# Optimization experiments

Measured on AMD Instinct MI355X. Metric: run time of the kernel, lower is better.

The kernel has to match this reference:

```python
import jax, jax.numpy as jnp
import numpy as np

B = 8192
NUM_CLASSES = 1024
DELTA = 0.2
GAMMA_1 = 10.0
GAMMA_2 = 0.5


def setup_inputs() -> dict:
    key = jax.random.key(0)
    k1, k2 = jax.random.split(key)
    scores = jax.random.uniform(k1, (B, B), dtype=jnp.float32)
    targets = jax.random.randint(k2, (B,), 0, NUM_CLASSES, dtype=jnp.int64)
    return {"scores": scores, "targets": targets}


def _side_loss(S, mask):
    # S: [B, B] similarities for this direction; mask: [B, B] bool, True = same label (positive)
    neg_mask = ~mask
    neg_inf = jnp.float32(-jnp.inf)
    pos_inf = jnp.float32(jnp.inf)
    max_an = jnp.max(jnp.where(neg_mask, S, neg_inf), axis=1)  # [B] hardest-negative score
    min_ap = jnp.min(jnp.where(mask, S, pos_inf), axis=1)      # [B] weakest-positive score
    # informative-pair filters (per row)
    ap_pair = mask & (S < (max_an + DELTA)[:, None])
    an_pair = neg_mask & (S > (min_ap - DELTA)[:, None])
    # masked exp-sums (log-sum-exp style margin terms)
    pos_sum = jnp.sum(jnp.where(ap_pair, jnp.exp(GAMMA_2 - GAMMA_1 * S), 0.0), axis=1)
    neg_sum = jnp.sum(jnp.where(an_pair, jnp.exp(GAMMA_1 * S - GAMMA_2), 0.0), axis=1)
    # safe log: rows with empty pair sets are marked invalid and zeroed later
    pos_loss = jnp.log(jnp.where(pos_sum > 0, pos_sum, 1.0)) / GAMMA_1
    neg_loss = jnp.log(jnp.where(neg_sum > 0, neg_sum, 1.0)) / GAMMA_1
    valid = jnp.any(ap_pair, axis=1) & jnp.any(an_pair, axis=1)
    return pos_loss + neg_loss, valid


def reference(scores, targets):
    batch_size = scores.shape[0]
    mask = targets[:, None] == targets[None, :]  # symmetric label-equality mask
    cap_loss, cap_valid = _side_loss(scores, mask)        # caption retrieval rows
    im_loss, im_valid = _side_loss(scores.T, mask)        # image retrieval rows (mask is symmetric)
    valid = cap_valid & im_valid  # original skips row if ANY of the 4 pair sets is empty
    loss = jnp.sum(jnp.where(valid, cap_loss + im_loss, 0.0)) / batch_size
    return loss
```

## Files before the change

### kernel.cpp

```cpp
#include <hip/hip_runtime.h>
#include <cmath>

#define BB 8192
#define NCH 64

static constexpr float kG1 = 10.0f;
static constexpr float kG2 = 0.5f;
static constexpr float kDelta = 0.2f;

__device__ __forceinline__ float wsum(float v){
#pragma unroll
  for (int o = 32; o > 0; o >>= 1) v += __shfl_xor(v, o);
  return v;
}
__device__ __forceinline__ float wmaxr(float v){
#pragma unroll
  for (int o = 32; o > 0; o >>= 1) v = fmaxf(v, __shfl_xor(v, o));
  return v;
}
__device__ __forceinline__ float wminr(float v){
#pragma unroll
  for (int o = 32; o > 0; o >>= 1) v = fminf(v, __shfl_xor(v, o));
  return v;
}


__global__ __launch_bounds__(256) void k_init(int* __restrict__ wsi, float* __restrict__ out){
  int i = blockIdx.x * 256 + threadIdx.x;
  if (i < 2*BB)      wsi[i] = (int)0xFF800000u;
  else if (i < 4*BB) wsi[i] = 0x7F800000;
  else if (i < 8*BB) reinterpret_cast<float*>(wsi)[i] = 0.0f;
  if (i == 0) out[0] = 0.0f;
}

__global__ __launch_bounds__(256) void k_row_stats(const float* __restrict__ S,
                                                   const int* __restrict__ tg,
                                                   int* __restrict__ row_max,
                                                   int* __restrict__ row_min){
  const int r = blockIdx.x;
  const int tr = tg[r];
  const float4* row = reinterpret_cast<const float4*>(S + (size_t)r * BB);
  const int4*  t4  = reinterpret_cast<const int4*>(tg);
  float mx = -INFINITY, mn = INFINITY;
  for (int it = threadIdx.x; it < BB/4; it += 256){
    float4 v = row[it];
    int4   t = t4[it];
    if (t.x == tr) mn = fminf(mn, v.x); else mx = fmaxf(mx, v.x);
    if (t.y == tr) mn = fminf(mn, v.y); else mx = fmaxf(mx, v.y);
    if (t.z == tr) mn = fminf(mn, v.z); else mx = fmaxf(mx, v.z);
    if (t.w == tr) mn = fminf(mn, v.w); else mx = fmaxf(mx, v.w);
  }
  mx = wmaxr(mx); mn = wminr(mn);
  __shared__ float smx[4], smn[4];
  const int wid = threadIdx.x >> 6;
  if ((threadIdx.x & 63) == 0){ smx[wid] = mx; smn[wid] = mn; }
  __syncthreads();
  if (threadIdx.x == 0){
    float a = smx[0], b = smn[0];
#pragma unroll
    for (int w = 1; w < 4; ++w){ a = fmaxf(a, smx[w]); b = fminf(b, smn[w]); }
    row_max[r] = __float_as_int(a);
    row_min[r] = __float_as_int(b);
  }
}

__global__ __launch_bounds__(256) void k_row_sums(const float* __restrict__ S,
                                                  const int* __restrict__ tg,
                                                  const int* __restrict__ row_max,
                                                  const int* __restrict__ row_min,
                                                  float* __restrict__ row_pos,
                                                  float* __restrict__ row_neg){
  const int r = blockIdx.x;
  const int tr = tg[r];
  const float pth = __int_as_float(row_max[r]) + kDelta;
  const float nth = __int_as_float(row_min[r]) - kDelta;
  const float4* row = reinterpret_cast<const float4*>(S + (size_t)r * BB);
  const int4*  t4  = reinterpret_cast<const int4*>(tg);
  float pos = 0.f, neg = 0.f;
  for (int it = threadIdx.x; it < BB/4; it += 256){
    float4 v = row[it];
    int4   t = t4[it];
    if (t.x == tr){ if (v.x < pth) pos += __expf(kG2 - kG1 * v.x); }
    else          { if (v.x > nth) neg += __expf(kG1 * v.x - kG2); }
    if (t.y == tr){ if (v.y < pth) pos += __expf(kG2 - kG1 * v.y); }
    else          { if (v.y > nth) neg += __expf(kG1 * v.y - kG2); }
    if (t.z == tr){ if (v.z < pth) pos += __expf(kG2 - kG1 * v.z); }
    else          { if (v.z > nth) neg += __expf(kG1 * v.z - kG2); }
    if (t.w == tr){ if (v.w < pth) pos += __expf(kG2 - kG1 * v.w); }
    else          { if (v.w > nth) neg += __expf(kG1 * v.w - kG2); }
  }
  pos = wsum(pos); neg = wsum(neg);
  __shared__ float sp[4], sn[4];
  const int wid = threadIdx.x >> 6;
  if ((threadIdx.x & 63) == 0){ sp[wid] = pos; sn[wid] = neg; }
  __syncthreads();
  if (threadIdx.x == 0){
    float a = sp[0], b = sn[0];
#pragma unroll
    for (int w = 1; w < 4; ++w){ a += sp[w]; b += sn[w]; }
    row_pos[r] = a; row_neg[r] = b;
  }
}

__global__ __launch_bounds__(256) void k_col_stats(const float* __restrict__ S,
                                                   const int* __restrict__ tg,
                                                   int* __restrict__ col_max,
                                                   int* __restrict__ col_min){
  const int c = (blockIdx.x * 256 + threadIdx.x) * 4;
  const int4 tc = *reinterpret_cast<const int4*>(tg + c);
  const int r0 = blockIdx.y * (BB / NCH);
  const int r1 = r0 + (BB / NCH);
  float mx0=-INFINITY, mx1=-INFINITY, mx2=-INFINITY, mx3=-INFINITY;
  float mn0= INFINITY, mn1= INFINITY, mn2= INFINITY, mn3= INFINITY;
  for (int i = r0; i < r1; ++i){
    float4 v = *reinterpret_cast<const float4*>(S + (size_t)i * BB + c);
    const int ti = tg[i];
    if (ti == tc.x) mn0 = fminf(mn0, v.x); else mx0 = fmaxf(mx0, v.x);
    if (ti == tc.y) mn1 = fminf(mn1, v.y); else mx1 = fmaxf(mx1, v.y);
    if (ti == tc.z) mn2 = fminf(mn2, v.z); else mx2 = fmaxf(mx2, v.z);
    if (ti == tc.w) mn3 = fminf(mn3, v.w); else mx3 = fmaxf(mx3, v.w);
  }
  atomicMax(col_max + c + 0, __float_as_int(mx0));
  atomicMax(col_max + c + 1, __float_as_int(mx1));
  atomicMax(col_max + c + 2, __float_as_int(mx2));
  atomicMax(col_max + c + 3, __float_as_int(mx3));
  atomicMin(col_min + c + 0, __float_as_int(mn0));
  atomicMin(col_min + c + 1, __float_as_int(mn1));
  atomicMin(col_min + c + 2, __float_as_int(mn2));
  atomicMin(col_min + c + 3, __float_as_int(mn3));
}

__global__ __launch_bounds__(256) void k_col_sums(const float* __restrict__ S,
                                                  const int* __restrict__ tg,
                                                  const int* __restrict__ col_max,
                                                  const int* __restrict__ col_min,
                                                  float* __restrict__ col_pos,
                                                  float* __restrict__ col_neg){
  const int c = (blockIdx.x * 256 + threadIdx.x) * 4;
  const int4 tc = *reinterpret_cast<const int4*>(tg + c);
  const float pth0 = __int_as_float(col_max[c+0]) + kDelta;
  const float pth1 = __int_as_float(col_max[c+1]) + kDelta;
  const float pth2 = __int_as_float(col_max[c+2]) + kDelta;
  const float pth3 = __int_as_float(col_max[c+3]) + kDelta;
  const float nth0 = __int_as_float(col_min[c+0]) - kDelta;
  const float nth1 = __int_as_float(col_min[c+1]) - kDelta;
  const float nth2 = __int_as_float(col_min[c+2]) - kDelta;
  const float nth3 = __int_as_float(col_min[c+3]) - kDelta;
  const int r0 = blockIdx.y * (BB / NCH);
  const int r1 = r0 + (BB / NCH);
  float p0=0.f,p1=0.f,p2=0.f,p3=0.f, n0=0.f,n1=0.f,n2=0.f,n3=0.f;
  for (int i = r0; i < r1; ++i){
    float4 v = *reinterpret_cast<const float4*>(S + (size_t)i * BB + c);
    const int ti = tg[i];
    if (ti == tc.x){ if (v.x < pth0) p0 += __expf(kG2 - kG1 * v.x); }
    else           { if (v.x > nth0) n0 += __expf(kG1 * v.x - kG2); }
    if (ti == tc.y){ if (v.y < pth1) p1 += __expf(kG2 - kG1 * v.y); }
    else           { if (v.y > nth1) n1 += __expf(kG1 * v.y - kG2); }
    if (ti == tc.z){ if (v.z < pth2) p2 += __expf(kG2 - kG1 * v.z); }
    else           { if (v.z > nth2) n2 += __expf(kG1 * v.z - kG2); }
    if (ti == tc.w){ if (v.w < pth3) p3 += __expf(kG2 - kG1 * v.w); }
    else           { if (v.w > nth3) n3 += __expf(kG1 * v.w - kG2); }
  }
  atomicAdd(col_pos + c + 0, p0);
  atomicAdd(col_pos + c + 1, p1);
  atomicAdd(col_pos + c + 2, p2);
  atomicAdd(col_pos + c + 3, p3);
  atomicAdd(col_neg + c + 0, n0);
  atomicAdd(col_neg + c + 1, n1);
  atomicAdd(col_neg + c + 2, n2);
  atomicAdd(col_neg + c + 3, n3);
}

__global__ __launch_bounds__(256) void k_final(const float* __restrict__ row_pos,
                                               const float* __restrict__ row_neg,
                                               const float* __restrict__ col_pos,
                                               const float* __restrict__ col_neg,
                                               float* __restrict__ out){
  const int r = blockIdx.x * 256 + threadIdx.x;
  const float rp = row_pos[r], rn = row_neg[r];
  const float cp = col_pos[r], cn = col_neg[r];
  float l = 0.f;
  if (rp > 0.f && rn > 0.f && cp > 0.f && cn > 0.f)
    l = (logf(rp) + logf(rn) + logf(cp) + logf(cn)) * (1.0f / kG1);
  l = wsum(l);
  __shared__ float sm[4];
  const int wid = threadIdx.x >> 6;
  if ((threadIdx.x & 63) == 0) sm[wid] = l;
  __syncthreads();
  if (threadIdx.x == 0){
    float a = sm[0] + sm[1] + sm[2] + sm[3];
    atomicAdd(out, a * (1.0f / (float)BB));
  }
}

extern "C" void kernel_launch(void* const* d_in, const int* in_sizes, int n_in,
                              void* d_out, int out_size, void* d_ws, size_t ws_size,
                              hipStream_t stream) {
  const float* S  = (const float*)d_in[0];
  const int*   tg = (const int*)d_in[1];
  int*   wsi = (int*)d_ws;
  float* wsf = (float*)d_ws;
  int* row_max = wsi;
  int* col_max = wsi + BB;
  int* row_min = wsi + 2*BB;
  int* col_min = wsi + 3*BB;
  float* row_pos = wsf + 4*BB;
  float* row_neg = wsf + 5*BB;
  float* col_pos = wsf + 6*BB;
  float* col_neg = wsf + 7*BB;
  float* out = (float*)d_out;

  k_init<<<(8*BB)/256, 256, 0, stream>>>(wsi, out);
  k_row_stats<<<BB, 256, 0, stream>>>(S, tg, row_max, row_min);
  k_col_stats<<<dim3(BB/1024, NCH), 256, 0, stream>>>(S, tg, col_max, col_min);
  k_row_sums<<<BB, 256, 0, stream>>>(S, tg, row_max, row_min, row_pos, row_neg);
  k_col_sums<<<dim3(BB/1024, NCH), 256, 0, stream>>>(S, tg, col_max, col_min, col_pos, col_neg);
  k_final<<<BB/256, 256, 0, stream>>>(row_pos, row_neg, col_pos, col_neg, out);
}
```

Before: 523.9 us.

## Fuse row and column passes into shared tiled stats and sums kernels

Merges the separate row-wise and column-wise stat and sum kernels into two tiled kernels that read each matrix element once per phase. Row reductions are done per row with a wave shuffle and combined across waves and blocks with atomics, while column reductions stay in registers. This halves the number of full passes over the 8192x8192 matrix, at the cost of per-row shuffle reductions and many more global atomics. The exponential is also computed once per element and shared between the row and column sums.

```diff
diff --git a/kernel.cpp b/kernel.cpp
--- a/kernel.cpp
+++ b/kernel.cpp
@@ -2,7 +2,9 @@
 #include <cmath>
 
 #define BB 8192
-#define NCH 64
+#define RPB 64
+#define GY (BB / RPB)
+#define GX (BB / 1024)
 
 static constexpr float kG1 = 10.0f;
 static constexpr float kG2 = 0.5f;
@@ -11,16 +13,6 @@
 __device__ __forceinline__ float wsum(float v){
 #pragma unroll
   for (int o = 32; o > 0; o >>= 1) v += __shfl_xor(v, o);
-  return v;
-}
-__device__ __forceinline__ float wmaxr(float v){
-#pragma unroll
-  for (int o = 32; o > 0; o >>= 1) v = fmaxf(v, __shfl_xor(v, o));
-  return v;
-}
-__device__ __forceinline__ float wminr(float v){
-#pragma unroll
-  for (int o = 32; o > 0; o >>= 1) v = fminf(v, __shfl_xor(v, o));
   return v;
 }
 
@@ -33,142 +25,145 @@
   if (i == 0) out[0] = 0.0f;
 }
 
-__global__ __launch_bounds__(256) void k_row_stats(const float* __restrict__ S,
-                                                   const int* __restrict__ tg,
-                                                   int* __restrict__ row_max,
-                                                   int* __restrict__ row_min){
-  const int r = blockIdx.x;
-  const int tr = tg[r];
-  const float4* row = reinterpret_cast<const float4*>(S + (size_t)r * BB);
-  const int4*  t4  = reinterpret_cast<const int4*>(tg);
-  float mx = -INFINITY, mn = INFINITY;
-  for (int it = threadIdx.x; it < BB/4; it += 256){
-    float4 v = row[it];
-    int4   t = t4[it];
-    if (t.x == tr) mn = fminf(mn, v.x); else mx = fmaxf(mx, v.x);
-    if (t.y == tr) mn = fminf(mn, v.y); else mx = fmaxf(mx, v.y);
-    if (t.z == tr) mn = fminf(mn, v.z); else mx = fmaxf(mx, v.z);
-    if (t.w == tr) mn = fminf(mn, v.w); else mx = fmaxf(mx, v.w);
-  }
-  mx = wmaxr(mx); mn = wminr(mn);
-  __shared__ float smx[4], smn[4];
-  const int wid = threadIdx.x >> 6;
-  if ((threadIdx.x & 63) == 0){ smx[wid] = mx; smn[wid] = mn; }
-  __syncthreads();
-  if (threadIdx.x == 0){
-    float a = smx[0], b = smn[0];
-#pragma unroll
-    for (int w = 1; w < 4; ++w){ a = fmaxf(a, smx[w]); b = fminf(b, smn[w]); }
-    row_max[r] = __float_as_int(a);
-    row_min[r] = __float_as_int(b);
-  }
-}
-
-__global__ __launch_bounds__(256) void k_row_sums(const float* __restrict__ S,
-                                                  const int* __restrict__ tg,
-                                                  const int* __restrict__ row_max,
-                                                  const int* __restrict__ row_min,
-                                                  float* __restrict__ row_pos,
-                                                  float* __restrict__ row_neg){
-  const int r = blockIdx.x;
-  const int tr = tg[r];
-  const float pth = __int_as_float(row_max[r]) + kDelta;
-  const float nth = __int_as_float(row_min[r]) - kDelta;
-  const float4* row = reinterpret_cast<const float4*>(S + (size_t)r * BB);
-  const int4*  t4  = reinterpret_cast<const int4*>(tg);
-  float pos = 0.f, neg = 0.f;
-  for (int it = threadIdx.x; it < BB/4; it += 256){
-    float4 v = row[it];
-    int4   t = t4[it];
-    if (t.x == tr){ if (v.x < pth) pos += __expf(kG2 - kG1 * v.x); }
-    else          { if (v.x > nth) neg += __expf(kG1 * v.x - kG2); }
-    if (t.y == tr){ if (v.y < pth) pos += __expf(kG2 - kG1 * v.y); }
-    else          { if (v.y > nth) neg += __expf(kG1 * v.y - kG2); }
-    if (t.z == tr){ if (v.z < pth) pos += __expf(kG2 - kG1 * v.z); }
-    else          { if (v.z > nth) neg += __expf(kG1 * v.z - kG2); }
-    if (t.w == tr){ if (v.w < pth) pos += __expf(kG2 - kG1 * v.w); }
-    else          { if (v.w > nth) neg += __expf(kG1 * v.w - kG2); }
-  }
-  pos = wsum(pos); neg = wsum(neg);
-  __shared__ float sp[4], sn[4];
-  const int wid = threadIdx.x >> 6;
-  if ((threadIdx.x & 63) == 0){ sp[wid] = pos; sn[wid] = neg; }
-  __syncthreads();
-  if (threadIdx.x == 0){
-    float a = sp[0], b = sn[0];
-#pragma unroll
-    for (int w = 1; w < 4; ++w){ a += sp[w]; b += sn[w]; }
-    row_pos[r] = a; row_neg[r] = b;
-  }
-}
-
-__global__ __launch_bounds__(256) void k_col_stats(const float* __restrict__ S,
-                                                   const int* __restrict__ tg,
-                                                   int* __restrict__ col_max,
-                                                   int* __restrict__ col_min){
+__global__ __launch_bounds__(256) void k_stats(const float* __restrict__ S,
+                                               const int* __restrict__ tg,
+                                               int* __restrict__ row_max,
+                                               int* __restrict__ row_min,
+                                               int* __restrict__ col_max,
+                                               int* __restrict__ col_min){
   const int c = (blockIdx.x * 256 + threadIdx.x) * 4;
   const int4 tc = *reinterpret_cast<const int4*>(tg + c);
-  const int r0 = blockIdx.y * (BB / NCH);
-  const int r1 = r0 + (BB / NCH);
-  float mx0=-INFINITY, mx1=-INFINITY, mx2=-INFINITY, mx3=-INFINITY;
-  float mn0= INFINITY, mn1= INFINITY, mn2= INFINITY, mn3= INFINITY;
-  for (int i = r0; i < r1; ++i){
-    float4 v = *reinterpret_cast<const float4*>(S + (size_t)i * BB + c);
-    const int ti = tg[i];
-    if (ti == tc.x) mn0 = fminf(mn0, v.x); else mx0 = fmaxf(mx0, v.x);
-    if (ti == tc.y) mn1 = fminf(mn1, v.y); else mx1 = fmaxf(mx1, v.y);
-    if (ti == tc.z) mn2 = fminf(mn2, v.z); else mx2 = fmaxf(mx2, v.z);
-    if (ti == tc.w) mn3 = fminf(mn3, v.w); else mx3 = fmaxf(mx3, v.w);
-  }
-  atomicMax(col_max + c + 0, __float_as_int(mx0));
-  atomicMax(col_max + c + 1, __float_as_int(mx1));
-  atomicMax(col_max + c + 2, __float_as_int(mx2));
-  atomicMax(col_max + c + 3, __float_as_int(mx3));
-  atomicMin(col_min + c + 0, __float_as_int(mn0));
-  atomicMin(col_min + c + 1, __float_as_int(mn1));
-  atomicMin(col_min + c + 2, __float_as_int(mn2));
-  atomicMin(col_min + c + 3, __float_as_int(mn3));
-}
-
-__global__ __launch_bounds__(256) void k_col_sums(const float* __restrict__ S,
-                                                  const int* __restrict__ tg,
-                                                  const int* __restrict__ col_max,
-                                                  const int* __restrict__ col_min,
-                                                  float* __restrict__ col_pos,
-                                                  float* __restrict__ col_neg){
+  const int r0 = blockIdx.y * RPB;
+  const int lane = threadIdx.x & 63;
+
+  float cmx0=-INFINITY, cmx1=-INFINITY, cmx2=-INFINITY, cmx3=-INFINITY;
+  float cmn0= INFINITY, cmn1= INFINITY, cmn2= INFINITY, cmn3= INFINITY;
+
+  __shared__ int s_t[RPB];
+  if (threadIdx.x < RPB) s_t[threadIdx.x] = tg[r0 + threadIdx.x];
+  __syncthreads();
+
+#pragma unroll 2
+  for (int k = 0; k < RPB; ++k){
+    const int i = r0 + k;
+    const float4 v = *reinterpret_cast<const float4*>(S + (size_t)i * BB + c);
+    const int ti = s_t[k];
+    float rmx = -INFINITY, rmn = INFINITY;
+    if (ti == tc.x){ cmn0 = fminf(cmn0, v.x); rmn = fminf(rmn, v.x); }
+    else           { cmx0 = fmaxf(cmx0, v.x); rmx = fmaxf(rmx, v.x); }
+    if (ti == tc.y){ cmn1 = fminf(cmn1, v.y); rmn = fminf(rmn, v.y); }
+    else           { cmx1 = fmaxf(cmx1, v.y); rmx = fmaxf(rmx, v.y); }
+    if (ti == tc.z){ cmn2 = fminf(cmn2, v.z); rmn = fminf(rmn, v.z); }
+    else           { cmx2 = fmaxf(cmx2, v.z); rmx = fmaxf(rmx, v.z); }
+    if (ti == tc.w){ cmn3 = fminf(cmn3, v.w); rmn = fminf(rmn, v.w); }
+    else           { cmx3 = fmaxf(cmx3, v.w); rmx = fmaxf(rmx, v.w); }
+#pragma unroll
+    for (int o = 32; o > 0; o >>= 1){
+      rmx = fmaxf(rmx, __shfl_xor(rmx, o));
+      rmn = fminf(rmn, __shfl_xor(rmn, o));
+    }
+    if (lane == 0){
+      atomicMax(row_max + i, __float_as_int(rmx));
+      atomicMin(row_min + i, __float_as_int(rmn));
+    }
+  }
+  atomicMax(col_max + c + 0, __float_as_int(cmx0));
+  atomicMax(col_max + c + 1, __float_as_int(cmx1));
+  atomicMax(col_max + c + 2, __float_as_int(cmx2));
+  atomicMax(col_max + c + 3, __float_as_int(cmx3));
+  atomicMin(col_min + c + 0, __float_as_int(cmn0));
+  atomicMin(col_min + c + 1, __float_as_int(cmn1));
+  atomicMin(col_min + c + 2, __float_as_int(cmn2));
+  atomicMin(col_min + c + 3, __float_as_int(cmn3));
+}
+
+__global__ __launch_bounds__(256) void k_sums(const float* __restrict__ S,
+                                              const int* __restrict__ tg,
+                                              const int* __restrict__ row_max,
+                                              const int* __restrict__ row_min,
+                                              const int* __restrict__ col_max,
+                                              const int* __restrict__ col_min,
+                                              float* __restrict__ row_pos,
+                                              float* __restrict__ row_neg,
+                                              float* __restrict__ col_pos,
+                                              float* __restrict__ col_neg){
   const int c = (blockIdx.x * 256 + threadIdx.x) * 4;
   const int4 tc = *reinterpret_cast<const int4*>(tg + c);
-  const float pth0 = __int_as_float(col_max[c+0]) + kDelta;
-  const float pth1 = __int_as_float(col_max[c+1]) + kDelta;
-  const float pth2 = __int_as_float(col_max[c+2]) + kDelta;
-  const float pth3 = __int_as_float(col_max[c+3]) + kDelta;
-  const float nth0 = __int_as_float(col_min[c+0]) - kDelta;
-  const float nth1 = __int_as_float(col_min[c+1]) - kDelta;
-  const float nth2 = __int_as_float(col_min[c+2]) - kDelta;
-  const float nth3 = __int_as_float(col_min[c+3]) - kDelta;
-  const int r0 = blockIdx.y * (BB / NCH);
-  const int r1 = r0 + (BB / NCH);
-  float p0=0.f,p1=0.f,p2=0.f,p3=0.f, n0=0.f,n1=0.f,n2=0.f,n3=0.f;
-  for (int i = r0; i < r1; ++i){
-    float4 v = *reinterpret_cast<const float4*>(S + (size_t)i * BB + c);
-    const int ti = tg[i];
-    if (ti == tc.x){ if (v.x < pth0) p0 += __expf(kG2 - kG1 * v.x); }
-    else           { if (v.x > nth0) n0 += __expf(kG1 * v.x - kG2); }
-    if (ti == tc.y){ if (v.y < pth1) p1 += __expf(kG2 - kG1 * v.y); }
-    else           { if (v.y > nth1) n1 += __expf(kG1 * v.y - kG2); }
-    if (ti == tc.z){ if (v.z < pth2) p2 += __expf(kG2 - kG1 * v.z); }
-    else           { if (v.z > nth2) n2 += __expf(kG1 * v.z - kG2); }
-    if (ti == tc.w){ if (v.w < pth3) p3 += __expf(kG2 - kG1 * v.w); }
-    else           { if (v.w > nth3) n3 += __expf(kG1 * v.w - kG2); }
-  }
-  atomicAdd(col_pos + c + 0, p0);
-  atomicAdd(col_pos + c + 1, p1);
-  atomicAdd(col_pos + c + 2, p2);
-  atomicAdd(col_pos + c + 3, p3);
-  atomicAdd(col_neg + c + 0, n0);
-  atomicAdd(col_neg + c + 1, n1);
-  atomicAdd(col_neg + c + 2, n2);
-  atomicAdd(col_neg + c + 3, n3);
+  const int r0 = blockIdx.y * RPB;
+  const int lane = threadIdx.x & 63;
+
+  const float cpth0 = __int_as_float(col_max[c+0]) + kDelta;
+  const float cpth1 = __int_as_float(col_max[c+1]) + kDelta;
+  const float cpth2 = __int_as_float(col_max[c+2]) + kDelta;
+  const float cpth3 = __int_as_float(col_max[c+3]) + kDelta;
+  const float cnth0 = __int_as_float(col_min[c+0]) - kDelta;
+  const float cnth1 = __int_as_float(col_min[c+1]) - kDelta;
+  const float cnth2 = __int_as_float(col_min[c+2]) - kDelta;
+  const float cnth3 = __int_as_float(col_min[c+3]) - kDelta;
+
+  __shared__ int   s_t[RPB];
+  __shared__ float s_pth[RPB], s_nth[RPB];
+  if (threadIdx.x < RPB){
+    const int i = r0 + threadIdx.x;
+    s_t[threadIdx.x]   = tg[i];
+    s_pth[threadIdx.x] = __int_as_float(row_max[i]) + kDelta;
+    s_nth[threadIdx.x] = __int_as_float(row_min[i]) - kDelta;
+  }
+  __syncthreads();
+
+  float cp0=0.f,cp1=0.f,cp2=0.f,cp3=0.f, cn0=0.f,cn1=0.f,cn2=0.f,cn3=0.f;
+
+#pragma unroll 2
+  for (int k = 0; k < RPB; ++k){
+    const int i = r0 + k;
+    const float4 v = *reinterpret_cast<const float4*>(S + (size_t)i * BB + c);
+    const int   ti  = s_t[k];
+    const float rpth = s_pth[k], rnth = s_nth[k];
+    float rp = 0.f, rn = 0.f;
+
+    {
+      const bool pos = (ti == tc.x);
+      const float arg = kG1 * v.x - kG2;
+      const float e = __expf(pos ? -arg : arg);
+      if (pos){ if (v.x < rpth) rp += e;  if (v.x < cpth0) cp0 += e; }
+      else    { if (v.x > rnth) rn += e;  if (v.x > cnth0) cn0 += e; }
+    }
+    {
+      const bool pos = (ti == tc.y);
+      const float arg = kG1 * v.y - kG2;
+      const float e = __expf(pos ? -arg : arg);
+      if (pos){ if (v.y < rpth) rp += e;  if (v.y < cpth1) cp1 += e; }
+      else    { if (v.y > rnth) rn += e;  if (v.y > cnth1) cn1 += e; }
+    }
+    {
+      const bool pos = (ti == tc.z);
+      const float arg = kG1 * v.z - kG2;
+      const float e = __expf(pos ? -arg : arg);
+      if (pos){ if (v.z < rpth) rp += e;  if (v.z < cpth2) cp2 += e; }
+      else    { if (v.z > rnth) rn += e;  if (v.z > cnth2) cn2 += e; }
+    }
+    {
+      const bool pos = (ti == tc.w);
+      const float arg = kG1 * v.w - kG2;
+      const float e = __expf(pos ? -arg : arg);
+      if (pos){ if (v.w < rpth) rp += e;  if (v.w < cpth3) cp3 += e; }
+      else    { if (v.w > rnth) rn += e;  if (v.w > cnth3) cn3 += e; }
+    }
+
+    rp = wsum(rp); rn = wsum(rn);
+    if (lane == 0){
+      atomicAdd(row_pos + i, rp);
+      atomicAdd(row_neg + i, rn);
+    }
+  }
+  atomicAdd(col_pos + c + 0, cp0);
+  atomicAdd(col_pos + c + 1, cp1);
+  atomicAdd(col_pos + c + 2, cp2);
+  atomicAdd(col_pos + c + 3, cp3);
+  atomicAdd(col_neg + c + 0, cn0);
+  atomicAdd(col_neg + c + 1, cn1);
+  atomicAdd(col_neg + c + 2, cn2);
+  atomicAdd(col_neg + c + 3, cn3);
 }
 
 __global__ __launch_bounds__(256) void k_final(const float* __restrict__ row_pos,
@@ -211,9 +206,8 @@
   float* out = (float*)d_out;
 
   k_init<<<(8*BB)/256, 256, 0, stream>>>(wsi, out);
-  k_row_stats<<<BB, 256, 0, stream>>>(S, tg, row_max, row_min);
-  k_col_stats<<<dim3(BB/1024, NCH), 256, 0, stream>>>(S, tg, col_max, col_min);
-  k_row_sums<<<BB, 256, 0, stream>>>(S, tg, row_max, row_min, row_pos, row_neg);
-  k_col_sums<<<dim3(BB/1024, NCH), 256, 0, stream>>>(S, tg, col_max, col_min, col_pos, col_neg);
+  k_stats<<<dim3(GX, GY), 256, 0, stream>>>(S, tg, row_max, row_min, col_max, col_min);
+  k_sums <<<dim3(GX, GY), 256, 0, stream>>>(S, tg, row_max, row_min, col_max, col_min,
+                                            row_pos, row_neg, col_pos, col_neg);
   k_final<<<BB/256, 256, 0, stream>>>(row_pos, row_neg, col_pos, col_neg, out);
 }
```

After: 476.9 us. 1.1x faster.
